# Performance work log

Hardware: AMD Instinct MI355X
Metric: run time of the kernel (lower is better)

Reference implementation:

```python
import jax, jax.numpy as jnp
import numpy as np

K = 3  # spatial kernel size (TVConv_k_square == 9)


def setup_inputs() -> dict:
    key = jax.random.key(0)
    k1, k2 = jax.random.split(key)
    B, C, H, W = 8, 96, 128, 128
    x = jax.random.normal(k1, (B, C, H, W), dtype=jnp.float32)
    weight_maps = jax.random.normal(k2, (1, C, K, K, H, W), dtype=jnp.float32)
    return {"x": x, "weight_maps": weight_maps}


def reference(x, weight_maps):
    # Per-pixel spatially-varying 3x3 depthwise conv.
    B, C, H, W = x.shape
    xp = jnp.pad(x, ((0, 0), (0, 0), (1, 1), (1, 1)))  # zero pad, (B,C,H+2,W+2)
    # Gather the 9 shifted views (equivalent to the as_strided unfold, stride 1).
    patches = jnp.stack(
        [xp[:, :, i:i + H, j:j + W] for i in range(K) for j in range(K)], axis=2
    ).reshape(B, C, K, K, H, W)
    # Weighted sum over the 3x3 window per channel per pixel.
    out = (weight_maps * patches).sum(axis=(2, 3))  # (B,C,H,W)
    return out
```

## Files before the change

### kernel.cpp

```cpp
#include <hip/hip_runtime.h>
#include <hip/hip_bf16.h>


namespace {
constexpr int B = 8, C = 96, H = 128, W = 128;
constexpr int HW = H * W;
constexpr int XROWS = 10;
constexpr int XB = XROWS * W * 4;
}

typedef __attribute__((address_space(1))) void gbl_void;
typedef __attribute__((address_space(3))) void lds_void;

__global__ __launch_bounds__(256, 3) void tvconv_kernel(
    const float* __restrict__ x,
    const float* __restrict__ wm,
    float* __restrict__ out) {
  __shared__ __align__(16) char xs[B * XB + 1024];

  const int t  = threadIdx.x;
  const int c  = blockIdx.x >> 4;
  const int h0 = (blockIdx.x & 15) * 8;
  const int lr = t >> 5;
  const int w4 = t & 31;
  const int h  = h0 + lr;
  const int w  = w4 * 4;

#pragma unroll
  for (int k = 0; k < 10; ++k) {
    const int i   = k * 256 + t;
    const int b   = i / 320;
    const int rem = i - b * 320;
    const int r   = rem >> 5;
    const int col = rem & 31;
    int row = h0 - 1 + r;
    row = min(max(row, 0), H - 1);
    const float* src = x + ((size_t)(b * C + c)) * HW + row * W + col * 4;
    __builtin_amdgcn_global_load_lds((const gbl_void*)src,
                                     (lds_void*)(xs + i * 16), 16, 0, 0);
  }

  const float* wp = wm + (size_t)c * 9 * HW + h * W + w;
  float4 wt[9];
#pragma unroll
  for (int k = 0; k < 9; ++k) {
    wt[k] = *reinterpret_cast<const float4*>(wp + (size_t)k * HW);
  }

  __syncthreads();

  const bool at_left  = (w4 == 0);
  const bool at_right = (w4 == 31);
  const bool top_pad  = (h == 0);
  const bool bot_pad  = (h == H - 1);
  const float4 zero4 = make_float4(0.f, 0.f, 0.f, 0.f);

#pragma unroll
  for (int b = 0; b < B; ++b) {
    float acc[4] = {0.f, 0.f, 0.f, 0.f};
#pragma unroll
    for (int i = 0; i < 3; ++i) {
      float4 ctr = *reinterpret_cast<const float4*>(
          xs + b * XB + (lr + i) * 512 + w4 * 16);
      const bool pad = (i == 0 && top_pad) || (i == 2 && bot_pad);
      if (pad) ctr = zero4;
      float left  = __shfl_up(ctr.w, 1);
      float right = __shfl_down(ctr.x, 1);
      if (at_left)  left  = 0.f;
      if (at_right) right = 0.f;
      const float xv[6] = {left, ctr.x, ctr.y, ctr.z, ctr.w, right};
#pragma unroll
      for (int j = 0; j < 3; ++j) {
        const float4 wv = wt[i * 3 + j];
        const float wa[4] = {wv.x, wv.y, wv.z, wv.w};
#pragma unroll
        for (int m = 0; m < 4; ++m) {
          acc[m] += wa[m] * xv[m + j];
        }
      }
    }
    float4 o;
    o.x = acc[0]; o.y = acc[1]; o.z = acc[2]; o.w = acc[3];
    *reinterpret_cast<float4*>(
        out + ((size_t)(b * C + c)) * HW + h * W + w) = o;
  }
}

extern "C" void kernel_launch(void* const* d_in, const int* in_sizes, int n_in,
                              void* d_out, int out_size, void* d_ws, size_t ws_size,
                              hipStream_t stream) {
  const float* x  = (const float*)d_in[0];
  const float* wm = (const float*)d_in[1];
  float* out = (float*)d_out;

  const int blocks = C * (H / 8);
  tvconv_kernel<<<blocks, 256, 0, stream>>>(x, wm, out);
}
```

Before: 140.8 us.

## Replace LDS staging with direct global row loads and raise occupancy

Drops the async global-to-LDS staging of the ten input rows per batch and the block barrier. Each thread now loads its three rows (up, center, down) straight from global memory per batch. Boundary rows are handled by zeroing the matching weight taps and clamping the row offsets. Removing the LDS footprint allows launch bounds to ask for 6 blocks per CU instead of 3. In exchange, each input row is read about three times through the cache instead of once into LDS.

```diff
diff --git a/kernel.cpp b/kernel.cpp
--- a/kernel.cpp
+++ b/kernel.cpp
@@ -1,23 +1,15 @@
 #include <hip/hip_runtime.h>
-#include <hip/hip_bf16.h>
 
 
 namespace {
 constexpr int B = 8, C = 96, H = 128, W = 128;
 constexpr int HW = H * W;
-constexpr int XROWS = 10;
-constexpr int XB = XROWS * W * 4;
 }
 
-typedef __attribute__((address_space(1))) void gbl_void;
-typedef __attribute__((address_space(3))) void lds_void;
-
-__global__ __launch_bounds__(256, 3) void tvconv_kernel(
+__global__ __launch_bounds__(256, 6) void tvconv_kernel(
     const float* __restrict__ x,
     const float* __restrict__ wm,
     float* __restrict__ out) {
-  __shared__ __align__(16) char xs[B * XB + 1024];
-
   const int t  = threadIdx.x;
   const int c  = blockIdx.x >> 4;
   const int h0 = (blockIdx.x & 15) * 8;
@@ -26,19 +18,7 @@
   const int h  = h0 + lr;
   const int w  = w4 * 4;
 
-#pragma unroll
-  for (int k = 0; k < 10; ++k) {
-    const int i   = k * 256 + t;
-    const int b   = i / 320;
-    const int rem = i - b * 320;
-    const int r   = rem >> 5;
-    const int col = rem & 31;
-    int row = h0 - 1 + r;
-    row = min(max(row, 0), H - 1);
-    const float* src = x + ((size_t)(b * C + c)) * HW + row * W + col * 4;
-    __builtin_amdgcn_global_load_lds((const gbl_void*)src,
-                                     (lds_void*)(xs + i * 16), 16, 0, 0);
-  }
+  const float4 zero4 = make_float4(0.f, 0.f, 0.f, 0.f);
 
   const float* wp = wm + (size_t)c * 9 * HW + h * W + w;
   float4 wt[9];
@@ -47,23 +27,28 @@
     wt[k] = *reinterpret_cast<const float4*>(wp + (size_t)k * HW);
   }
 
-  __syncthreads();
+  if (h == 0)     { wt[0] = zero4; wt[1] = zero4; wt[2] = zero4; }
+  if (h == H - 1) { wt[6] = zero4; wt[7] = zero4; wt[8] = zero4; }
+  const int up = (h == 0)     ? 0 : W;
+  const int dn = (h == H - 1) ? 0 : W;
 
   const bool at_left  = (w4 == 0);
   const bool at_right = (w4 == 31);
-  const bool top_pad  = (h == 0);
-  const bool bot_pad  = (h == H - 1);
-  const float4 zero4 = make_float4(0.f, 0.f, 0.f, 0.f);
+
+  const float* xb = x   + (size_t)c * HW + h * W + w;
+  float*       ob = out + (size_t)c * HW + h * W + w;
 
 #pragma unroll
   for (int b = 0; b < B; ++b) {
+    const float4 r0 = *reinterpret_cast<const float4*>(xb - up);
+    const float4 r1 = *reinterpret_cast<const float4*>(xb);
+    const float4 r2 = *reinterpret_cast<const float4*>(xb + dn);
+    const float4 rows[3] = {r0, r1, r2};
+
     float acc[4] = {0.f, 0.f, 0.f, 0.f};
 #pragma unroll
     for (int i = 0; i < 3; ++i) {
-      float4 ctr = *reinterpret_cast<const float4*>(
-          xs + b * XB + (lr + i) * 512 + w4 * 16);
-      const bool pad = (i == 0 && top_pad) || (i == 2 && bot_pad);
-      if (pad) ctr = zero4;
+      const float4 ctr = rows[i];
       float left  = __shfl_up(ctr.w, 1);
       float right = __shfl_down(ctr.x, 1);
       if (at_left)  left  = 0.f;
@@ -81,8 +66,10 @@
     }
     float4 o;
     o.x = acc[0]; o.y = acc[1]; o.z = acc[2]; o.w = acc[3];
-    *reinterpret_cast<float4*>(
-        out + ((size_t)(b * C + c)) * HW + h * W + w) = o;
+    *reinterpret_cast<float4*>(ob) = o;
+
+    xb += (size_t)C * HW;
+    ob += (size_t)C * HW;
   }
 }
 
```

Result: no change. 140.9 us (+0.1%).
